# Optimization experiments

Measured on AMD Instinct MI355X. Metric: run time of the kernel, lower is better.

The kernel has to match this reference:

```python
import jax, jax.numpy as jnp
import numpy as np

THETA = 10000.0
R_TOK = 4  # region_token_num


def _local_positions(regions, max_n):
    # 0-based position of each token within its region (count of prior tokens
    # with the same region id) -- order-based, works for any region layout.
    onehot = jax.nn.one_hot(regions, max_n + 1, dtype=jnp.int32)  # [B,T,N+1]
    counts = jnp.cumsum(onehot, axis=1)                            # inclusive
    return jnp.take_along_axis(counts, regions[..., None], axis=-1)[..., 0] - 1


def _rope(q, k, pos, theta):
    # full-head-dim rotary embedding, split-half convention
    D = q.shape[-1]
    inv_freq = 1.0 / (theta ** (jnp.arange(0, D, 2, dtype=jnp.float32) / D))  # [D/2]
    ang = pos[..., None].astype(jnp.float32) * inv_freq                        # [B,S,D/2]
    cos = jnp.tile(jnp.cos(ang), (1, 1, 2))[:, None]                           # [B,1,S,D]
    sin = jnp.tile(jnp.sin(ang), (1, 1, 2))[:, None]

    def rot(x):
        h = x.shape[-1] // 2
        return jnp.concatenate([-x[..., h:], x[..., :h]], axis=-1)

    return q * cos + rot(q) * sin, k * cos + rot(k) * sin


def setup_inputs() -> dict:
    B, H, D = 2, 16, 64
    T, MAX_N = 2048, 64
    P = MAX_N * R_TOK
    key = jax.random.key(0)
    ks = jax.random.split(key, 7)
    f = lambda k, s: jax.random.normal(k, s, dtype=jnp.float32)
    regions = jnp.sort(jax.random.randint(ks[6], (B, T), 1, MAX_N + 1, dtype=jnp.int32), axis=-1)
    return {
        'pool_q': f(ks[0], (B, H, P, D)),
        'pool_k': f(ks[1], (B, H, P, D)),
        'pool_v': f(ks[2], (B, H, P, D)),
        'x_q': f(ks[3], (B, H, T, D)),
        'x_k': f(ks[4], (B, H, T, D)),
        'x_v': f(ks[5], (B, H, T, D)),
        'regions': regions,
        't_mask': jnp.ones((B, T), dtype=bool),
        'n_mask': jnp.ones((B, MAX_N), dtype=bool),
        'max_n': MAX_N,
    }


def reference(pool_q, pool_k, pool_v, x_q, x_k, x_v, regions, t_mask, n_mask, max_n):
    B, H, P, D = pool_q.shape
    R = R_TOK
    # sequence = [pool, x]
    q = jnp.concatenate([pool_q, x_q], axis=2)
    k = jnp.concatenate([pool_k, x_k], axis=2)
    v = jnp.concatenate([pool_v, x_v], axis=2)

    # local-mode positions (use_pool_offset=False -> pool tokens at pos 0)
    pool_pos = jnp.zeros((B, P), dtype=jnp.int32)
    x_pos = (_local_positions(regions, max_n) + R) * (regions > 0).astype(jnp.int32)
    pos = jnp.concatenate([pool_pos, x_pos], axis=-1)  # [B,S]
    q, k = _rope(q, k, pos, THETA)

    # block-local (same-region) mask: [B,1,S,S], True = allowed
    pool_region = jnp.broadcast_to(jnp.repeat(jnp.arange(1, max_n + 1, dtype=jnp.int32), R)[None], (B, P))
    pool_valid = jnp.repeat(n_mask, R, axis=1)                      # [B,P]
    full_region = jnp.concatenate([pool_region, regions], axis=-1)  # [B,S]
    full_valid = jnp.concatenate([pool_valid, t_mask], axis=-1)     # [B,S]
    same = full_region[:, :, None] == full_region[:, None, :]
    valid = full_valid[:, :, None] & full_valid[:, None, :]
    nonpad = (full_region != 0)[:, :, None] & (full_region != 0)[:, None, :]
    mask = (same & valid & nonpad)[:, None]                          # [B,1,S,S]

    scores = jnp.einsum('bhqd,bhkd->bhqk', q, k) / jnp.sqrt(jnp.float32(D))
    scores = jnp.where(mask, scores, jnp.float32(-1e9))
    attn = jax.nn.softmax(scores, axis=-1)
    out = jnp.einsum('bhqk,bhkd->bhqd', attn, v)
    return out[:, :, :P, :]
```

## Files before the change

### kernel.cpp

```cpp
#include <hip/hip_runtime.h>
#include <hip/hip_bf16.h>

#define BB   2
#define HH   16
#define DD   64
#define TT   2048
#define MAXN 64
#define RTOK 4
#define PP   (MAXN * RTOK)
#define KPAD 65

__global__ __launch_bounds__(256, 4)
void lapd_attn(const float* __restrict__ pool_q,
               const float* __restrict__ pool_k,
               const float* __restrict__ pool_v,
               const float* __restrict__ x_k,
               const float* __restrict__ x_v,
               const int* __restrict__ regions,
               float* __restrict__ out) {
    const int blk   = blockIdx.x;
    const int r_idx = blk & (MAXN - 1);
    const int bh    = blk >> 6;
    const int r     = r_idx + 1;
    const int b     = bh / HH;

    const int tid  = threadIdx.x;
    const int wave = tid >> 6;
    const int lane = tid & 63;

    __shared__ float k_s[64][KPAD];
    __shared__ float v_s[64][KPAD];
    __shared__ float q_s[4][DD];
    __shared__ float p_s[4][64];
    __shared__ int   cnt_s[4];

    const size_t poolbase = ((size_t)bh * PP + r_idx * RTOK) * DD;
    const float* pk = pool_k + poolbase;
    const float* pv = pool_v + poolbase;
    const float* xk = x_k + (size_t)bh * TT * DD;
    const float* xv = x_v + (size_t)bh * TT * DD;

    const size_t qidx = poolbase + (size_t)(wave * DD) + lane;
    const float qv = pool_q[qidx] * 0.125f;
    q_s[wave][lane] = qv;

    {
        const int4* reg4 = (const int4*)(regions + b * TT);
        int c_lt = 0, c_le = 0;
        #pragma unroll
        for (int i = 0; i < 2; ++i) {
            const int4 v = reg4[tid + i * 256];
            c_lt += (v.x <  r) + (v.y <  r) + (v.z <  r) + (v.w <  r);
            c_le += (v.x <= r) + (v.y <= r) + (v.z <= r) + (v.w <= r);
        }
        int packed = c_lt | (c_le << 16);
        #pragma unroll
        for (int off = 32; off > 0; off >>= 1)
            packed += __shfl_xor(packed, off, 64);
        if (lane == 0) cnt_s[wave] = packed;
    }
    __syncthreads();
    const int tot    = cnt_s[0] + cnt_s[1] + cnt_s[2] + cnt_s[3];
    const int start  = tot & 0xFFFF;
    const int n_keys = ((tot >> 16) & 0xFFFF) - start + RTOK;

    float m = -1e30f, l = 0.0f, acc = 0.0f;

    for (int tile = 0; tile < n_keys; tile += 64) {
        const int tn = min(64, n_keys - tile);
        __syncthreads();

        float4 kvb[4], kpb[4], vvb[4];
        #pragma unroll
        for (int p = 0; p < 4; ++p) {
            const int flat = p * 1024 + tid * 4;
            if (flat < tn * DD) {
                const int key = flat >> 6;
                const int dim = flat & 63;
                const int gk  = tile + key;
                if (gk < RTOK) {
                    kvb[p] = *(const float4*)(pk + gk * DD + dim);
                    kpb[p] = kvb[p];
                    vvb[p] = *(const float4*)(pv + gk * DD + dim);
                } else {
                    const size_t off = (size_t)(start + gk - RTOK) * DD;
                    kvb[p] = *(const float4*)(xk + off + dim);
                    kpb[p] = *(const float4*)(xk + off + ((dim + 32) & 63));
                    vvb[p] = *(const float4*)(xv + off + dim);
                }
            }
        }
        #pragma unroll
        for (int p = 0; p < 4; ++p) {
            const int flat = p * 1024 + tid * 4;
            if (flat < tn * DD) {
                const int key = flat >> 6;
                const int dim = flat & 63;
                const int gk  = tile + key;
                float kr[4] = {kvb[p].x, kvb[p].y, kvb[p].z, kvb[p].w};
                if (gk >= RTOK) {
                    const float pos = (float)gk;
                    const float sgn = (dim < 32) ? -1.0f : 1.0f;
                    const float kpd[4] = {kpb[p].x, kpb[p].y, kpb[p].z, kpb[p].w};
                    #pragma unroll
                    for (int c = 0; c < 4; ++c) {
                        const int j = (dim + c) & 31;
                        const float invf = __expf((float)j * (-9.210340371976184f / 32.0f));
                        float sv, cv;
                        __sincosf(pos * invf, &sv, &cv);
                        kr[c] = kr[c] * cv + sgn * kpd[c] * sv;
                    }
                }
                k_s[key][dim + 0] = kr[0];
                k_s[key][dim + 1] = kr[1];
                k_s[key][dim + 2] = kr[2];
                k_s[key][dim + 3] = kr[3];
                v_s[key][dim + 0] = vvb[p].x;
                v_s[key][dim + 1] = vvb[p].y;
                v_s[key][dim + 2] = vvb[p].z;
                v_s[key][dim + 3] = vvb[p].w;
            }
        }
        __syncthreads();

        float s = -1e30f;
        if (lane < tn) {
            float s0 = 0, s1 = 0, s2 = 0, s3 = 0;
            #pragma unroll
            for (int d = 0; d < DD; d += 4) {
                s0 += q_s[wave][d + 0] * k_s[lane][d + 0];
                s1 += q_s[wave][d + 1] * k_s[lane][d + 1];
                s2 += q_s[wave][d + 2] * k_s[lane][d + 2];
                s3 += q_s[wave][d + 3] * k_s[lane][d + 3];
            }
            s = (s0 + s1) + (s2 + s3);
        }
        float tm = s;
        #pragma unroll
        for (int off = 32; off > 0; off >>= 1)
            tm = fmaxf(tm, __shfl_xor(tm, off, 64));
        const float m_new = fmaxf(m, tm);
        const float alpha = __expf(m - m_new);
        const float p = (lane < tn) ? __expf(s - m_new) : 0.0f;
        float ts = p;
        #pragma unroll
        for (int off = 32; off > 0; off >>= 1)
            ts += __shfl_xor(ts, off, 64);
        l = l * alpha + ts;
        m = m_new;
        p_s[wave][lane] = p;

        acc *= alpha;
        float a0 = 0, a1 = 0, a2 = 0, a3 = 0;
        int k = 0;
        for (; k + 3 < tn; k += 4) {
            a0 += p_s[wave][k + 0] * v_s[k + 0][lane];
            a1 += p_s[wave][k + 1] * v_s[k + 1][lane];
            a2 += p_s[wave][k + 2] * v_s[k + 2][lane];
            a3 += p_s[wave][k + 3] * v_s[k + 3][lane];
        }
        for (; k < tn; ++k)
            acc += p_s[wave][k] * v_s[k][lane];
        acc += (a0 + a1) + (a2 + a3);
    }

    out[qidx] = acc / l;
}

extern "C" void kernel_launch(void* const* d_in, const int* in_sizes, int n_in,
                              void* d_out, int out_size, void* d_ws, size_t ws_size,
                              hipStream_t stream) {
    const float* pool_q  = (const float*)d_in[0];
    const float* pool_k  = (const float*)d_in[1];
    const float* pool_v  = (const float*)d_in[2];
    const float* x_k     = (const float*)d_in[4];
    const float* x_v     = (const float*)d_in[5];
    const int*   regions = (const int*)d_in[6];
    float*       out     = (float*)d_out;

    lapd_attn<<<dim3(BB * HH * MAXN), dim3(256), 0, stream>>>(
        pool_q, pool_k, pool_v, x_k, x_v, regions, out);
}
```

Before: 119.6 us.

## Precompute region ranges in a prepass kernel and restructure K/V staging

Adds a small kernel that builds per-batch region start offsets from the sorted region ids, so each attention block reads its range directly instead of counting over all tokens. K/V staging moves into a helper that gets the rotate-half partner via a lane shuffle instead of a second global load, stores V transposed, and uses float4 shared-memory reads in the dot products. The PV loop is fully unrolled to 64 keys, with unused slots zeroed or given p=0. The prepass relies on sorted regions, and the extra launch adds its own overhead.

```diff
diff --git a/kernel.cpp b/kernel.cpp
--- a/kernel.cpp
+++ b/kernel.cpp
@@ -8,7 +8,76 @@
 #define MAXN 64
 #define RTOK 4
 #define PP   (MAXN * RTOK)
-#define KPAD 65
+#define PAD  68
+
+__global__ __launch_bounds__(256)
+void build_ranges(const int* __restrict__ regions, int* __restrict__ tab) {
+    const int b   = blockIdx.x;
+    const int tid = threadIdx.x;
+    const int* reg = regions + b * TT;
+    int* t = tab + b * 66;
+    const int i0 = tid * 8;
+    int v[9];
+    const int4 a0 = *(const int4*)(reg + i0);
+    const int4 a1 = *(const int4*)(reg + i0 + 4);
+    v[0] = a0.x; v[1] = a0.y; v[2] = a0.z; v[3] = a0.w;
+    v[4] = a1.x; v[5] = a1.y; v[6] = a1.z; v[7] = a1.w;
+    v[8] = (tid == 255) ? (MAXN + 1) : reg[i0 + 8];
+    if (tid == 0)
+        for (int rr = 1; rr <= v[0]; ++rr) t[rr] = 0;
+    #pragma unroll
+    for (int j = 0; j < 8; ++j)
+        for (int rr = v[j] + 1; rr <= v[j + 1]; ++rr) t[rr] = i0 + j + 1;
+}
+
+__device__ __forceinline__ void stage_x(const float* __restrict__ xk,
+                                        const float* __restrict__ xv,
+                                        int start, int xbase, int nx, int koff,
+                                        int nrows, int tid,
+                                        float (*k_s)[PAD], float (*v_t)[PAD]) {
+    float4 kv[4], vv[4];
+    int dim[4], xi_u[4];
+    #pragma unroll
+    for (int p = 0; p < 4; ++p) {
+        const int flat = p * 1024 + tid * 4;
+        xi_u[p] = flat >> 6;
+        dim[p]  = flat & 63;
+        const int xi = min(xi_u[p], nx - 1);
+        const size_t off = (size_t)(start + xbase + xi) * DD;
+        kv[p] = *(const float4*)(xk + off + dim[p]);
+        vv[p] = *(const float4*)(xv + off + dim[p]);
+    }
+    #pragma unroll
+    for (int p = 0; p < 4; ++p) {
+        float4 kp;
+        kp.x = __shfl_xor(kv[p].x, 8, 64);
+        kp.y = __shfl_xor(kv[p].y, 8, 64);
+        kp.z = __shfl_xor(kv[p].z, 8, 64);
+        kp.w = __shfl_xor(kv[p].w, 8, 64);
+        const int key = koff + xi_u[p];
+        if (key < 64) {
+            const int d = dim[p];
+            const float pos = (float)(xbase + xi_u[p] + RTOK);
+            const float sgn = (d < 32) ? -1.0f : 1.0f;
+            const float kd[4]  = {kv[p].x, kv[p].y, kv[p].z, kv[p].w};
+            const float kpd[4] = {kp.x, kp.y, kp.z, kp.w};
+            float kr[4];
+            #pragma unroll
+            for (int c = 0; c < 4; ++c) {
+                const int j = (d + c) & 31;
+                const float invf = __expf((float)j * (-9.210340371976184f / 32.0f));
+                float sv, cv;
+                __sincosf(pos * invf, &sv, &cv);
+                kr[c] = kd[c] * cv + sgn * kpd[c] * sv;
+            }
+            *(float4*)&k_s[key][d] = make_float4(kr[0], kr[1], kr[2], kr[3]);
+            v_t[d + 0][key] = vv[p].x;
+            v_t[d + 1][key] = vv[p].y;
+            v_t[d + 2][key] = vv[p].z;
+            v_t[d + 3][key] = vv[p].w;
+        }
+    }
+}
 
 __global__ __launch_bounds__(256, 4)
 void lapd_attn(const float* __restrict__ pool_q,
@@ -16,23 +85,25 @@
                const float* __restrict__ pool_v,
                const float* __restrict__ x_k,
                const float* __restrict__ x_v,
-               const int* __restrict__ regions,
+               const int* __restrict__ tab,
                float* __restrict__ out) {
     const int blk   = blockIdx.x;
     const int r_idx = blk & (MAXN - 1);
     const int bh    = blk >> 6;
-    const int r     = r_idx + 1;
     const int b     = bh / HH;
 
     const int tid  = threadIdx.x;
     const int wave = tid >> 6;
     const int lane = tid & 63;
 
-    __shared__ float k_s[64][KPAD];
-    __shared__ float v_s[64][KPAD];
+    __shared__ float k_s[64][PAD];
+    __shared__ float v_t[64][PAD];
     __shared__ float q_s[4][DD];
     __shared__ float p_s[4][64];
-    __shared__ int   cnt_s[4];
+
+    const int* tb   = tab + b * 66;
+    const int start = tb[r_idx + 1];
+    const int cnt   = tb[r_idx + 2] - start;
 
     const size_t poolbase = ((size_t)bh * PP + r_idx * RTOK) * DD;
     const float* pk = pool_k + poolbase;
@@ -44,83 +115,36 @@
     const float qv = pool_q[qidx] * 0.125f;
     q_s[wave][lane] = qv;
 
-    {
-        const int4* reg4 = (const int4*)(regions + b * TT);
-        int c_lt = 0, c_le = 0;
-        #pragma unroll
-        for (int i = 0; i < 2; ++i) {
-            const int4 v = reg4[tid + i * 256];
-            c_lt += (v.x <  r) + (v.y <  r) + (v.z <  r) + (v.w <  r);
-            c_le += (v.x <= r) + (v.y <= r) + (v.z <= r) + (v.w <= r);
-        }
-        int packed = c_lt | (c_le << 16);
-        #pragma unroll
-        for (int off = 32; off > 0; off >>= 1)
-            packed += __shfl_xor(packed, off, 64);
-        if (lane == 0) cnt_s[wave] = packed;
-    }
-    __syncthreads();
-    const int tot    = cnt_s[0] + cnt_s[1] + cnt_s[2] + cnt_s[3];
-    const int start  = tot & 0xFFFF;
-    const int n_keys = ((tot >> 16) & 0xFFFF) - start + RTOK;
+    if (tid < 64) {
+        const int key = tid >> 4, d = (tid & 15) * 4;
+        const float4 kvp = *(const float4*)(pk + key * DD + d);
+        const float4 vvp = *(const float4*)(pv + key * DD + d);
+        *(float4*)&k_s[key][d] = kvp;
+        v_t[d + 0][key] = vvp.x;
+        v_t[d + 1][key] = vvp.y;
+        v_t[d + 2][key] = vvp.z;
+        v_t[d + 3][key] = vvp.w;
+    }
+
+    int tn, xbase;
+    if (cnt > 0) {
+        const int nx0 = min(cnt, 60);
+        stage_x(xk, xv, start, 0, nx0, RTOK, 60, tid, k_s, v_t);
+        tn = RTOK + nx0;
+        xbase = nx0;
+    } else {
+        for (int i = tid; i < 60 * DD; i += 256) {
+            const int key = 4 + (i >> 6), d = i & 63;
+            k_s[key][d] = 0.0f;
+            v_t[d][key] = 0.0f;
+        }
+        tn = RTOK;
+        xbase = 0;
+    }
 
     float m = -1e30f, l = 0.0f, acc = 0.0f;
 
-    for (int tile = 0; tile < n_keys; tile += 64) {
-        const int tn = min(64, n_keys - tile);
-        __syncthreads();
-
-        float4 kvb[4], kpb[4], vvb[4];
-        #pragma unroll
-        for (int p = 0; p < 4; ++p) {
-            const int flat = p * 1024 + tid * 4;
-            if (flat < tn * DD) {
-                const int key = flat >> 6;
-                const int dim = flat & 63;
-                const int gk  = tile + key;
-                if (gk < RTOK) {
-                    kvb[p] = *(const float4*)(pk + gk * DD + dim);
-                    kpb[p] = kvb[p];
-                    vvb[p] = *(const float4*)(pv + gk * DD + dim);
-                } else {
-                    const size_t off = (size_t)(start + gk - RTOK) * DD;
-                    kvb[p] = *(const float4*)(xk + off + dim);
-                    kpb[p] = *(const float4*)(xk + off + ((dim + 32) & 63));
-                    vvb[p] = *(const float4*)(xv + off + dim);
-                }
-            }
-        }
-        #pragma unroll
-        for (int p = 0; p < 4; ++p) {
-            const int flat = p * 1024 + tid * 4;
-            if (flat < tn * DD) {
-                const int key = flat >> 6;
-                const int dim = flat & 63;
-                const int gk  = tile + key;
-                float kr[4] = {kvb[p].x, kvb[p].y, kvb[p].z, kvb[p].w};
-                if (gk >= RTOK) {
-                    const float pos = (float)gk;
-                    const float sgn = (dim < 32) ? -1.0f : 1.0f;
-                    const float kpd[4] = {kpb[p].x, kpb[p].y, kpb[p].z, kpb[p].w};
-                    #pragma unroll
-                    for (int c = 0; c < 4; ++c) {
-                        const int j = (dim + c) & 31;
-                        const float invf = __expf((float)j * (-9.210340371976184f / 32.0f));
-                        float sv, cv;
-                        __sincosf(pos * invf, &sv, &cv);
-                        kr[c] = kr[c] * cv + sgn * kpd[c] * sv;
-                    }
-                }
-                k_s[key][dim + 0] = kr[0];
-                k_s[key][dim + 1] = kr[1];
-                k_s[key][dim + 2] = kr[2];
-                k_s[key][dim + 3] = kr[3];
-                v_s[key][dim + 0] = vvb[p].x;
-                v_s[key][dim + 1] = vvb[p].y;
-                v_s[key][dim + 2] = vvb[p].z;
-                v_s[key][dim + 3] = vvb[p].w;
-            }
-        }
+    for (;;) {
         __syncthreads();
 
         float s = -1e30f;
@@ -128,10 +152,11 @@
             float s0 = 0, s1 = 0, s2 = 0, s3 = 0;
             #pragma unroll
             for (int d = 0; d < DD; d += 4) {
-                s0 += q_s[wave][d + 0] * k_s[lane][d + 0];
-                s1 += q_s[wave][d + 1] * k_s[lane][d + 1];
-                s2 += q_s[wave][d + 2] * k_s[lane][d + 2];
-                s3 += q_s[wave][d + 3] * k_s[lane][d + 3];
+                const float4 kk = *(const float4*)&k_s[lane][d];
+                s0 += q_s[wave][d + 0] * kk.x;
+                s1 += q_s[wave][d + 1] * kk.y;
+                s2 += q_s[wave][d + 2] * kk.z;
+                s3 += q_s[wave][d + 3] * kk.w;
             }
             s = (s0 + s1) + (s2 + s3);
         }
@@ -152,16 +177,22 @@
 
         acc *= alpha;
         float a0 = 0, a1 = 0, a2 = 0, a3 = 0;
-        int k = 0;
-        for (; k + 3 < tn; k += 4) {
-            a0 += p_s[wave][k + 0] * v_s[k + 0][lane];
-            a1 += p_s[wave][k + 1] * v_s[k + 1][lane];
-            a2 += p_s[wave][k + 2] * v_s[k + 2][lane];
-            a3 += p_s[wave][k + 3] * v_s[k + 3][lane];
-        }
-        for (; k < tn; ++k)
-            acc += p_s[wave][k] * v_s[k][lane];
+        #pragma unroll
+        for (int k = 0; k < 64; k += 4) {
+            const float4 vv4 = *(const float4*)&v_t[lane][k];
+            a0 += p_s[wave][k + 0] * vv4.x;
+            a1 += p_s[wave][k + 1] * vv4.y;
+            a2 += p_s[wave][k + 2] * vv4.z;
+            a3 += p_s[wave][k + 3] * vv4.w;
+        }
         acc += (a0 + a1) + (a2 + a3);
+
+        if (xbase >= cnt) break;
+        __syncthreads();
+        const int nx = min(64, cnt - xbase);
+        stage_x(xk, xv, start, xbase, nx, 0, 64, tid, k_s, v_t);
+        tn = nx;
+        xbase += nx;
     }
 
     out[qidx] = acc / l;
@@ -177,7 +208,9 @@
     const float* x_v     = (const float*)d_in[5];
     const int*   regions = (const int*)d_in[6];
     float*       out     = (float*)d_out;
-
+    int*         tab     = (int*)d_ws;
+
+    build_ranges<<<dim3(BB), dim3(256), 0, stream>>>(regions, tab);
     lapd_attn<<<dim3(BB * HH * MAXN), dim3(256), 0, stream>>>(
-        pool_q, pool_k, pool_v, x_k, x_v, regions, out);
-}
+        pool_q, pool_k, pool_v, x_k, x_v, tab, out);
+}
```

Measured after the change: 114.4 us. 1.05x faster.
